# Optimization experiments

Measured on AMD Instinct MI355X. Metric: run time of the kernel, lower is better.

Reference implementation:

```python
import jax, jax.numpy as jnp
import numpy as np

B, L, IN_DIM, D, H, NCONV = 64, 400, 500, 128, 8, 4
HD = D // H  # head dim = 16


def _conv1d(x, w, b, pad, groups=1):
    # x: [B, L, Cin], w: [k, Cin//groups, Cout]
    y = jax.lax.conv_general_dilated(
        x, w, window_strides=(1,), padding=[(pad, pad)],
        dimension_numbers=('NWC', 'WIO', 'NWC'), feature_group_count=groups)
    return y + b


def _layernorm(x, g, b, eps=1e-5):
    mu = jnp.mean(x, axis=-1, keepdims=True)
    var = jnp.mean(jnp.square(x - mu), axis=-1, keepdims=True)
    return (x - mu) * jax.lax.rsqrt(var + eps) * g + b


def _posenc(L, d):
    pos = jnp.arange(L, dtype=jnp.float32)[:, None]                 # [L,1]
    div = jnp.exp(jnp.arange(0, d, 2, dtype=jnp.float32) * (-jnp.log(10000.0) / d))
    ang = pos * div                                                 # [L, d/2]
    return jnp.stack([jnp.sin(ang), jnp.cos(ang)], axis=-1).reshape(L, d)


def setup_inputs() -> dict:
    key = jax.random.key(0)
    ks = jax.random.split(key, 24)
    s = lambda k, shape, scale: jax.random.normal(k, shape, dtype=jnp.float32) * scale
    inp = {
        'x': s(ks[0], (B, L, IN_DIM), 1.0),
        # init conv: k=5, 500 -> 128
        'w_init': s(ks[1], (5, IN_DIM, D), 0.02),
        'b_init': jnp.zeros((D,), jnp.float32),
        # 4 depthwise-separable conv layers (pre-LN, residual): depthwise k=7
        'ln_conv_g': jnp.ones((NCONV, D), jnp.float32),
        'ln_conv_b': jnp.zeros((NCONV, D), jnp.float32),
        'w_dw': s(ks[2], (NCONV, 7, 1, D), 0.1),
        'b_dw': jnp.zeros((NCONV, D), jnp.float32),
        'w_pw': s(ks[3], (NCONV, 1, D, D), 0.05),
        'b_pw': jnp.zeros((NCONV, D), jnp.float32),
        # self-attention (pre-LN, residual)
        'ln_att_g': jnp.ones((D,), jnp.float32),
        'ln_att_b': jnp.zeros((D,), jnp.float32),
        'wq': s(ks[4], (D, D), 0.05), 'bq': jnp.zeros((D,), jnp.float32),
        'wk': s(ks[5], (D, D), 0.05), 'bk': jnp.zeros((D,), jnp.float32),
        'wv': s(ks[6], (D, D), 0.05), 'bv': jnp.zeros((D,), jnp.float32),
        'wo': s(ks[7], (D, D), 0.05), 'bo': jnp.zeros((D,), jnp.float32),
        # FFN (pre-LN, residual)
        'ln_ffn_g': jnp.ones((D,), jnp.float32),
        'ln_ffn_b': jnp.zeros((D,), jnp.float32),
        'w1': s(ks[8], (D, D), 0.05), 'b1': jnp.zeros((D,), jnp.float32),
        'w2': s(ks[9], (D, D), 0.05), 'b2': jnp.zeros((D,), jnp.float32),
    }
    return inp


def reference(x, w_init, b_init, ln_conv_g, ln_conv_b, w_dw, b_dw, w_pw, b_pw,
              ln_att_g, ln_att_b, wq, bq, wk, bk, wv, bv, wo, bo,
              ln_ffn_g, ln_ffn_b, w1, b1, w2, b2):
    # 1) init conv (Conv1d k=5 pad=2, 500 -> 128); torch permutes, equivalent NWC conv
    h = _conv1d(x, w_init, b_init, pad=2)                    # [B, L, D]
    # 2) positional encoding
    h = h + _posenc(h.shape[1], D)
    for i in range(NCONV):
        res = h
        h = _layernorm(h, ln_conv_g[i], ln_conv_b[i])
        h = _conv1d(h, w_dw[i], b_dw[i], pad=3, groups=D)    # depthwise k=7
        h = _conv1d(h, w_pw[i], b_pw[i], pad=0)              # pointwise 1x1
        h = jax.nn.relu(h) + res
    # 4) multi-head self-attention, pre-LN + residual
    res = h
    hn = _layernorm(h, ln_att_g, ln_att_b)
    q = (hn @ wq + bq).reshape(B, L, H, HD)
    k = (hn @ wk + bk).reshape(B, L, H, HD)
    v = (hn @ wv + bv).reshape(B, L, H, HD)
    scores = jnp.einsum('bqhd,bkhd->bhqk', q, k) / jnp.sqrt(jnp.float32(HD))
    attn = jax.nn.softmax(scores, axis=-1)
    o = jnp.einsum('bhqk,bkhd->bqhd', attn, v).reshape(B, L, D)
    h = o @ wo + bo + res
    # 5) FFN, pre-LN + residual
    res = h
    hn = _layernorm(h, ln_ffn_g, ln_ffn_b)
    h = jax.nn.relu(hn @ w1 + b1) @ w2 + b2 + res
    return h
```

## Files before the change

### kernel.cpp

```cpp
#include <hip/hip_runtime.h>
#include <hip/hip_bf16.h>
#include <math.h>

#define B 64
#define L 400
#define IN_DIM 500
#define D 128
#define H 8
#define HD 16
#define NCONV 4
#define BL (B*L)

typedef __attribute__((ext_vector_type(8))) unsigned short ushort8;
typedef __attribute__((ext_vector_type(8))) short bf16x8;
typedef __attribute__((ext_vector_type(4))) float f32x4;

__device__ __forceinline__ unsigned short f2bf(float f) {
    unsigned u = __float_as_uint(f);
    unsigned r = (u + 0x7fffu + ((u >> 16) & 1u)) >> 16;
    return (unsigned short)r;
}
__device__ __forceinline__ float bf2f(unsigned short u) {
    return __uint_as_float(((unsigned)u) << 16);
}

__device__ __forceinline__ void gload16(const void* g, void* l) {
    __builtin_amdgcn_global_load_lds(
        (const __attribute__((address_space(1))) unsigned int*)g,
        (__attribute__((address_space(3))) unsigned int*)l,
        16, 0, 0);
}

__global__ __launch_bounds__(256) void k_cvt_x(
        const float* __restrict__ x, unsigned short* __restrict__ xb) {
    int idx = blockIdx.x * 256 + threadIdx.x;
    int row = idx >> 6, ch = idx & 63;
    int b = row / 404, rr = row - b * 404;
    ushort8 o = (ushort8)0;
    if (rr >= 2 && rr < 402) {
        int l = rr - 2;
        const float* src = x + ((size_t)b * 400 + l) * 500 + ch * 8;
        if (ch < 62) {
            float4 v0 = *(const float4*)(src);
            float4 v1 = *(const float4*)(src + 4);
            o[0] = f2bf(v0.x); o[1] = f2bf(v0.y); o[2] = f2bf(v0.z); o[3] = f2bf(v0.w);
            o[4] = f2bf(v1.x); o[5] = f2bf(v1.y); o[6] = f2bf(v1.z); o[7] = f2bf(v1.w);
        } else {
#pragma unroll
            for (int j = 0; j < 8; ++j) {
                int c = ch * 8 + j;
                o[j] = (c < 500) ? f2bf(src[j]) : (unsigned short)0;
            }
        }
    }
    *(ushort8*)(xb + (size_t)idx * 8) = o;
}

__global__ __launch_bounds__(256) void k_cvt_w(
        const float* __restrict__ w, unsigned short* __restrict__ wbt) {
    int idx = blockIdx.x * 256 + threadIdx.x;
    int k = idx & 511, n = (idx >> 9) & 127, t = idx >> 16;
    float v = (k < 500) ? w[((size_t)t * 500 + k) * 128 + n] : 0.f;
    wbt[idx] = f2bf(v);
}

__global__ __launch_bounds__(256) void k_cvt_wall(
        const float* w0, const float* w1, const float* w2, const float* w3,
        const float* w4, const float* w5, const float* w6, const float* w7,
        const float* w8, const float* w9, unsigned short* __restrict__ out) {
    const float* arr[10] = {w0,w1,w2,w3,w4,w5,w6,w7,w8,w9};
    int widx = blockIdx.x >> 6;
    const float* w = arr[widx];
    int idx = ((blockIdx.x & 63) << 8) + threadIdx.x;
    int n = idx >> 7, k = idx & 127;
    out[(size_t)widx * 16384 + idx] = f2bf(w[k * 128 + n]);
}

#define TM 80
#define BK 64
__global__ __launch_bounds__(256) void k_initconv_mfma(
        const unsigned short* __restrict__ xb,
        const unsigned short* __restrict__ wbt,
        const float* __restrict__ bias, float* __restrict__ out) {
    __shared__ unsigned short As[TM * BK];
    __shared__ unsigned short Ws[64 * BK];
    int tid = threadIdx.x;
    int b = blockIdx.x / 10;
    int rem = blockIdx.x - b * 10;
    int l0 = (rem >> 1) * TM;
    int nh = rem & 1;
    int lane = tid & 63, wave = tid >> 6;
    int kgrp = lane >> 4, lm = lane & 15;

    f32x4 acc[5];
#pragma unroll
    for (int mf = 0; mf < 5; ++mf) acc[mf] = (f32x4)0.f;

    for (int t = 0; t < 5; ++t) {
        const unsigned short* arow = xb + ((size_t)(b * 404 + l0 + t)) * 512;
        const unsigned short* wrow = wbt + (size_t)t * 128 * 512 + (size_t)nh * 64 * 512;
        for (int k0 = 0; k0 < 512; k0 += BK) {
            {
                int idx = tid;
#pragma unroll
                for (int i = 0; i < 2; ++i) {
                    int r = idx >> 3, sc = idx & 7;
                    gload16(arow + (size_t)r * 512 + k0 + ((sc ^ (r & 7)) * 8),
                            As + idx * 8);
                    idx += 256;
                }
                if (idx < 640) {
                    int r = idx >> 3, sc = idx & 7;
                    gload16(arow + (size_t)r * 512 + k0 + ((sc ^ (r & 7)) * 8),
                            As + idx * 8);
                }
            }
#pragma unroll
            for (int i = 0; i < 2; ++i) {
                int idx = tid + i * 256;
                int n = idx >> 3, sc = idx & 7;
                gload16(wrow + (size_t)n * 512 + k0 + ((sc ^ (n & 7)) * 8),
                        Ws + idx * 8);
            }
            __syncthreads();
#pragma unroll
            for (int ks = 0; ks < 2; ++ks) {
                int gc = ks * 4 + kgrp;
                int n = wave * 16 + lm;
                bf16x8 bfr = *(const bf16x8*)(Ws + n * 64 + ((gc ^ (n & 7)) * 8));
#pragma unroll
                for (int mf = 0; mf < 5; ++mf) {
                    int r = mf * 16 + lm;
                    bf16x8 af = *(const bf16x8*)(As + r * 64 + ((gc ^ (r & 7)) * 8));
                    acc[mf] = __builtin_amdgcn_mfma_f32_16x16x32_bf16(
                        af, bfr, acc[mf], 0, 0, 0);
                }
            }
            __syncthreads();
        }
    }

    {
        int n = nh * 64 + wave * 16 + lm;
        float bs = bias[n];
        float pbase = expf(-(float)(n & ~1) * (9.210340371976184f / 128.0f));
#pragma unroll
        for (int mf = 0; mf < 5; ++mf) {
#pragma unroll
            for (int r = 0; r < 4; ++r) {
                int l = l0 + mf * 16 + kgrp * 4 + r;
                float ang = (float)l * pbase;
                float pe = (n & 1) ? cosf(ang) : sinf(ang);
                out[((size_t)b * 400 + l) * 128 + n] = acc[mf][r] + bs + pe;
            }
        }
    }
}

__global__ __launch_bounds__(256) void k_ln(
        const float* __restrict__ in, const float* __restrict__ g,
        const float* __restrict__ bta, unsigned short* __restrict__ out) {
    int wave = threadIdx.x >> 6, lane = threadIdx.x & 63;
    size_t row = (size_t)blockIdx.x * 4 + wave;
    const float* p = in + row * D;
    float2 v = *(const float2*)(p + lane * 2);
    float s = v.x + v.y;
    float q = v.x * v.x + v.y * v.y;
#pragma unroll
    for (int off = 32; off; off >>= 1) {
        s += __shfl_xor(s, off);
        q += __shfl_xor(q, off);
    }
    float mu  = s * (1.f / 128.f);
    float var = q * (1.f / 128.f) - mu * mu;
    float inv = rsqrtf(var + 1e-5f);
    float2 gg = *(const float2*)(g + lane * 2);
    float2 bb = *(const float2*)(bta + lane * 2);
    float ox = (v.x - mu) * inv * gg.x + bb.x;
    float oy = (v.y - mu) * inv * gg.y + bb.y;
    unsigned pk = (unsigned)f2bf(ox) | ((unsigned)f2bf(oy) << 16);
    *(unsigned*)(out + row * D + lane * 2) = pk;
}

__global__ __launch_bounds__(256) void k_dw(
        const unsigned short* __restrict__ in, const float* __restrict__ w,
        const float* __restrict__ bias, unsigned short* __restrict__ out) {
    __shared__ float s[22 * D];
    int tid = threadIdx.x;
    int b  = blockIdx.x / 25;
    int l0 = (blockIdx.x - b * 25) * 16;
    for (int idx = tid; idx < 22 * 16; idx += 256) {
        int r = idx >> 4, c = idx & 15;
        int gl = l0 - 3 + r;
        float vals[8];
        if (gl >= 0 && gl < L) {
            ushort8 u = *(const ushort8*)(in + ((size_t)b * L + gl) * D + c * 8);
#pragma unroll
            for (int j = 0; j < 8; ++j) vals[j] = bf2f(u[j]);
        } else {
#pragma unroll
            for (int j = 0; j < 8; ++j) vals[j] = 0.f;
        }
#pragma unroll
        for (int j = 0; j < 8; ++j) s[r * D + c * 8 + j] = vals[j];
    }
    __syncthreads();
    int d = tid & 127, half = tid >> 7;
    float wr[7];
#pragma unroll
    for (int t = 0; t < 7; ++t) wr[t] = w[t * D + d];
    float bs = bias[d];
    for (int jj = 0; jj < 8; ++jj) {
        int lj = half * 8 + jj;
        float a = bs;
#pragma unroll
        for (int t = 0; t < 7; ++t) a = fmaf(s[(lj + t) * D + d], wr[t], a);
        out[((size_t)b * L + l0 + lj) * D + d] = f2bf(a);
    }
}

__global__ __launch_bounds__(256) void k_gemm_bf16(
        const unsigned short* __restrict__ A,
        const unsigned short* __restrict__ Wt,
        const float* __restrict__ bias,
        const float* __restrict__ res,
        float* __restrict__ outf,
        unsigned short* __restrict__ outb,
        int relu, float oscale) {
    __shared__ unsigned short As[32 * 128];
    __shared__ unsigned short Ws[128 * 128];
    int tid = threadIdx.x;
    int m0 = blockIdx.x * 32;
    int lane = tid & 63, wave = tid >> 6;
    int lm = lane & 15, kgrp = lane >> 4;
    int wm = wave >> 1, wn = wave & 1;

#pragma unroll
    for (int i = 0; i < 2; ++i) {
        int idx = tid + i * 256;
        int r = idx >> 4, sc = idx & 15;
        gload16(A + ((size_t)(m0 + r)) * 128 + ((sc ^ (r & 15)) * 8), As + idx * 8);
    }
#pragma unroll
    for (int i = 0; i < 8; ++i) {
        int idx = tid + i * 256;
        int n = idx >> 4, sc = idx & 15;
        gload16(Wt + ((size_t)n) * 128 + ((sc ^ (n & 15)) * 8), Ws + idx * 8);
    }
    __syncthreads();

    f32x4 acc[4];
#pragma unroll
    for (int nt = 0; nt < 4; ++nt) acc[nt] = (f32x4)0.f;

#pragma unroll
    for (int kc = 0; kc < 4; ++kc) {
        int c = kc * 4 + kgrp;
        int r = wm * 16 + lm;
        bf16x8 af = *(const bf16x8*)(As + (r * 16 + (c ^ (r & 15))) * 8);
#pragma unroll
        for (int nt = 0; nt < 4; ++nt) {
            int n = wn * 64 + nt * 16 + lm;
            bf16x8 bfv = *(const bf16x8*)(Ws + (n * 16 + (c ^ (n & 15))) * 8);
            acc[nt] = __builtin_amdgcn_mfma_f32_16x16x32_bf16(af, bfv, acc[nt], 0, 0, 0);
        }
    }

#pragma unroll
    for (int nt = 0; nt < 4; ++nt) {
        int n = wn * 64 + nt * 16 + lm;
        float bs = bias[n];
#pragma unroll
        for (int r = 0; r < 4; ++r) {
            size_t m = (size_t)m0 + wm * 16 + kgrp * 4 + r;
            float v = acc[nt][r] + bs;
            if (relu) v = fmaxf(v, 0.f);
            if (res)  v += res[m * 128 + n];
            if (outf) outf[m * 128 + n] = v;
            else      outb[m * 128 + n] = f2bf(v * oscale);
        }
    }
}

#define KS 40
#define VS 424
__global__ __launch_bounds__(256) void k_attn_mfma(
        const unsigned short* __restrict__ qb,
        const unsigned short* __restrict__ kb,
        const unsigned short* __restrict__ vb,
        unsigned short* __restrict__ out) {
    __shared__ __align__(16) unsigned short Kpad[400 * KS];
    __shared__ __align__(16) unsigned short Vt[16 * VS];
    __shared__ __align__(16) unsigned short Ptmp[4][16 * KS];
    int tid = threadIdx.x;
    int b = blockIdx.x >> 3, h = blockIdx.x & 7;
    int lane = tid & 63, wave = tid >> 6;
    int lm = lane & 15, kgrp = lane >> 4;

    for (int idx = tid; idx < 800; idx += 256) {
        int l = idx >> 1, half = idx & 1;
        ushort8 kv = *(const ushort8*)(kb + ((size_t)(b * 400 + l)) * 128 + h * 16 + half * 8);
        *(ushort8*)(Kpad + l * KS + half * 8) = kv;
        *(ushort8*)(Kpad + l * KS + 16 + half * 8) = (ushort8)0;
    }
    for (int idx = tid; idx < 800; idx += 256) {
        int kk = idx >> 1, dh = idx & 1;
        ushort8 vv = *(const ushort8*)(vb + ((size_t)(b * 400 + kk)) * 128 + h * 16 + dh * 8);
#pragma unroll
        for (int j = 0; j < 8; ++j) Vt[(dh * 8 + j) * VS + kk] = vv[j];
    }
    {
        int d = tid >> 4, kk = 400 + (tid & 15);
        Vt[d * VS + kk] = 0;
    }
    __syncthreads();

    unsigned short* Pw = Ptmp[wave];
    for (int tt = wave; tt < 25; tt += 4) {
        int q0 = tt * 16;
        bf16x8 Qf = *(const bf16x8*)(qb + ((size_t)(b * 400 + q0 + lm)) * 128 + h * 16 + kgrp * 8);
        f32x4 s[25];
#pragma unroll
        for (int kt = 0; kt < 25; ++kt) {
            bf16x8 Kf = *(const bf16x8*)(Kpad + (kt * 16 + lm) * KS + kgrp * 8);
            s[kt] = __builtin_amdgcn_mfma_f32_16x16x32_bf16(Qf, Kf, (f32x4)0.f, 0, 0, 0);
        }
        float rmax[4], rsum[4];
#pragma unroll
        for (int r = 0; r < 4; ++r) rmax[r] = -1e30f;
#pragma unroll
        for (int kt = 0; kt < 25; ++kt)
#pragma unroll
            for (int r = 0; r < 4; ++r) rmax[r] = fmaxf(rmax[r], s[kt][r]);
#pragma unroll
        for (int mask = 1; mask <= 8; mask <<= 1)
#pragma unroll
            for (int r = 0; r < 4; ++r) rmax[r] = fmaxf(rmax[r], __shfl_xor(rmax[r], mask));
#pragma unroll
        for (int r = 0; r < 4; ++r) rsum[r] = 0.f;
#pragma unroll
        for (int kt = 0; kt < 25; ++kt)
#pragma unroll
            for (int r = 0; r < 4; ++r) {
                float p = __expf(s[kt][r] - rmax[r]);
                s[kt][r] = p;
                rsum[r] += p;
            }
#pragma unroll
        for (int mask = 1; mask <= 8; mask <<= 1)
#pragma unroll
            for (int r = 0; r < 4; ++r) rsum[r] += __shfl_xor(rsum[r], mask);
        float rinv[4];
#pragma unroll
        for (int r = 0; r < 4; ++r) rinv[r] = 1.f / rsum[r];

        f32x4 O = (f32x4)0.f;
#pragma unroll
        for (int kc = 0; kc < 13; ++kc) {
#pragma unroll
            for (int t = 0; t < 2; ++t) {
                int kt = kc * 2 + t;
#pragma unroll
                for (int r = 0; r < 4; ++r) {
                    unsigned short pv = (kt < 25) ? f2bf(s[kt][r]) : (unsigned short)0;
                    Pw[(kgrp * 4 + r) * KS + t * 16 + lm] = pv;
                }
            }
            __builtin_amdgcn_wave_barrier();
            __builtin_amdgcn_s_waitcnt(0);
            __builtin_amdgcn_wave_barrier();
            bf16x8 Pf = *(const bf16x8*)(Pw + lm * KS + kgrp * 8);
            bf16x8 Vf = *(const bf16x8*)(Vt + lm * VS + kc * 32 + kgrp * 8);
            O = __builtin_amdgcn_mfma_f32_16x16x32_bf16(Pf, Vf, O, 0, 0, 0);
            __builtin_amdgcn_wave_barrier();
        }
#pragma unroll
        for (int r = 0; r < 4; ++r) {
            int q = q0 + kgrp * 4 + r;
            out[((size_t)(b * 400 + q)) * 128 + h * 16 + lm] = f2bf(O[r] * rinv[r]);
        }
    }
}

extern "C" void kernel_launch(void* const* d_in, const int* in_sizes, int n_in,
                              void* d_out, int out_size, void* d_ws, size_t ws_size,
                              hipStream_t stream) {
    (void)in_sizes; (void)n_in; (void)out_size; (void)ws_size;
    const float* x      = (const float*)d_in[0];
    const float* w_init = (const float*)d_in[1];
    const float* b_init = (const float*)d_in[2];
    const float* lncg   = (const float*)d_in[3];
    const float* lncb   = (const float*)d_in[4];
    const float* w_dw   = (const float*)d_in[5];
    const float* b_dw   = (const float*)d_in[6];
    const float* w_pw   = (const float*)d_in[7];
    const float* b_pw   = (const float*)d_in[8];
    const float* lnag   = (const float*)d_in[9];
    const float* lnab   = (const float*)d_in[10];
    const float* wq     = (const float*)d_in[11];
    const float* bq     = (const float*)d_in[12];
    const float* wk     = (const float*)d_in[13];
    const float* bk     = (const float*)d_in[14];
    const float* wv     = (const float*)d_in[15];
    const float* bv     = (const float*)d_in[16];
    const float* wo     = (const float*)d_in[17];
    const float* bo     = (const float*)d_in[18];
    const float* lnfg   = (const float*)d_in[19];
    const float* lnfb   = (const float*)d_in[20];
    const float* w1     = (const float*)d_in[21];
    const float* b1     = (const float*)d_in[22];
    const float* w2     = (const float*)d_in[23];
    const float* b2     = (const float*)d_in[24];

    float* ws = (float*)d_ws;
    const size_t NBL = (size_t)BL * D;
    float* h0 = ws;
    float* outp = (float*)d_out;

    unsigned short* hnb = (unsigned short*)(ws + NBL);
    unsigned short* t0b = hnb + NBL;
    unsigned short* qb  = t0b + NBL;
    unsigned short* kb  = qb + NBL;
    unsigned short* vb  = kb + NBL;
    unsigned short* wt  = vb + NBL;
    unsigned short* xb  = wt + 10 * 16384;
    unsigned short* wbt = xb + (size_t)64 * 404 * 512;

    k_cvt_x<<<6464, 256, 0, stream>>>(x, xb);
    k_cvt_w<<<1280, 256, 0, stream>>>(w_init, wbt);
    k_cvt_wall<<<640, 256, 0, stream>>>(
        w_pw, w_pw + 16384, w_pw + 2 * 16384, w_pw + 3 * 16384,
        wq, wk, wv, wo, w1, w2, wt);

    k_initconv_mfma<<<640, 256, 0, stream>>>(xb, wbt, b_init, h0);

    for (int i = 0; i < NCONV; ++i) {
        k_ln<<<6400, 256, 0, stream>>>(h0, lncg + i * D, lncb + i * D, hnb);
        k_dw<<<1600, 256, 0, stream>>>(hnb, w_dw + (size_t)i * 7 * D, b_dw + i * D, t0b);
        k_gemm_bf16<<<800, 256, 0, stream>>>(t0b, wt + (size_t)i * 16384,
                                             b_pw + i * D, h0, h0, nullptr, 1, 1.f);
    }

    k_ln<<<6400, 256, 0, stream>>>(h0, lnag, lnab, hnb);
    k_gemm_bf16<<<800, 256, 0, stream>>>(hnb, wt + 4 * 16384, bq, nullptr,
                                         nullptr, qb, 0, 0.25f);
    k_gemm_bf16<<<800, 256, 0, stream>>>(hnb, wt + 5 * 16384, bk, nullptr,
                                         nullptr, kb, 0, 1.f);
    k_gemm_bf16<<<800, 256, 0, stream>>>(hnb, wt + 6 * 16384, bv, nullptr,
                                         nullptr, vb, 0, 1.f);
    k_attn_mfma<<<512, 256, 0, stream>>>(qb, kb, vb, t0b);
    k_gemm_bf16<<<800, 256, 0, stream>>>(t0b, wt + 7 * 16384, bo, h0,
                                         h0, nullptr, 0, 1.f);

    k_ln<<<6400, 256, 0, stream>>>(h0, lnfg, lnfb, hnb);
    k_gemm_bf16<<<800, 256, 0, stream>>>(hnb, wt + 8 * 16384, b1, nullptr,
                                         nullptr, t0b, 1, 1.f);
    k_gemm_bf16<<<800, 256, 0, stream>>>(t0b, wt + 9 * 16384, b2, h0,
                                         outp, nullptr, 0, 1.f);
}
```

Before: 381.7 us.

## Reuse one 84-row input tile across all five conv taps in init conv

```diff
diff --git a/kernel.cpp b/kernel.cpp
--- a/kernel.cpp
+++ b/kernel.cpp
@@ -82,8 +82,8 @@
         const unsigned short* __restrict__ xb,
         const unsigned short* __restrict__ wbt,
         const float* __restrict__ bias, float* __restrict__ out) {
-    __shared__ unsigned short As[TM * BK];
-    __shared__ unsigned short Ws[64 * BK];
+    __shared__ unsigned short As[84 * BK];
+    __shared__ unsigned short Ws[5][64 * BK];
     int tid = threadIdx.x;
     int b = blockIdx.x / 10;
     int rem = blockIdx.x - b * 10;
@@ -96,48 +96,48 @@
 #pragma unroll
     for (int mf = 0; mf < 5; ++mf) acc[mf] = (f32x4)0.f;
 
-    for (int t = 0; t < 5; ++t) {
-        const unsigned short* arow = xb + ((size_t)(b * 404 + l0 + t)) * 512;
-        const unsigned short* wrow = wbt + (size_t)t * 128 * 512 + (size_t)nh * 64 * 512;
-        for (int k0 = 0; k0 < 512; k0 += BK) {
-            {
-                int idx = tid;
-#pragma unroll
-                for (int i = 0; i < 2; ++i) {
-                    int r = idx >> 3, sc = idx & 7;
-                    gload16(arow + (size_t)r * 512 + k0 + ((sc ^ (r & 7)) * 8),
-                            As + idx * 8);
-                    idx += 256;
-                }
-                if (idx < 640) {
-                    int r = idx >> 3, sc = idx & 7;
-                    gload16(arow + (size_t)r * 512 + k0 + ((sc ^ (r & 7)) * 8),
-                            As + idx * 8);
+    const unsigned short* abase = xb + ((size_t)(b * 404 + l0)) * 512;
+    const unsigned short* wbase = wbt + (size_t)nh * 64 * 512;
+
+    for (int k0 = 0; k0 < 512; k0 += BK) {
+        for (int idx = tid; idx < 672; idx += 256) {
+            int r = idx >> 3, sc = idx & 7;
+            gload16(abase + (size_t)r * 512 + k0 + ((sc ^ (r & 7)) * 8),
+                    As + idx * 8);
+        }
+#pragma unroll
+        for (int i = 0; i < 10; ++i) {
+            int idx = tid + i * 256;
+            int t = idx >> 9;
+            int sub = idx & 511;
+            int n = sub >> 3, sc = sub & 7;
+            gload16(wbase + (size_t)t * 128 * 512 + (size_t)n * 512 + k0
+                        + ((sc ^ (n & 7)) * 8),
+                    &Ws[t][0] + sub * 8);
+        }
+        __syncthreads();
+        int n16 = wave * 16 + lm;
+#pragma unroll
+        for (int ks = 0; ks < 2; ++ks) {
+            int gc = ks * 4 + kgrp;
+            bf16x8 bfr[5];
+#pragma unroll
+            for (int t = 0; t < 5; ++t)
+                bfr[t] = *(const bf16x8*)(&Ws[t][0] + n16 * 64
+                                          + ((gc ^ (n16 & 7)) * 8));
+#pragma unroll
+            for (int mf = 0; mf < 5; ++mf) {
+#pragma unroll
+                for (int t = 0; t < 5; ++t) {
+                    int r = mf * 16 + lm + t;
+                    bf16x8 af = *(const bf16x8*)(As + r * 64
+                                                 + ((gc ^ (r & 7)) * 8));
+                    acc[mf] = __builtin_amdgcn_mfma_f32_16x16x32_bf16(
+                        af, bfr[t], acc[mf], 0, 0, 0);
                 }
             }
-#pragma unroll
-            for (int i = 0; i < 2; ++i) {
-                int idx = tid + i * 256;
-                int n = idx >> 3, sc = idx & 7;
-                gload16(wrow + (size_t)n * 512 + k0 + ((sc ^ (n & 7)) * 8),
-                        Ws + idx * 8);
-            }
-            __syncthreads();
-#pragma unroll
-            for (int ks = 0; ks < 2; ++ks) {
-                int gc = ks * 4 + kgrp;
-                int n = wave * 16 + lm;
-                bf16x8 bfr = *(const bf16x8*)(Ws + n * 64 + ((gc ^ (n & 7)) * 8));
-#pragma unroll
-                for (int mf = 0; mf < 5; ++mf) {
-                    int r = mf * 16 + lm;
-                    bf16x8 af = *(const bf16x8*)(As + r * 64 + ((gc ^ (r & 7)) * 8));
-                    acc[mf] = __builtin_amdgcn_mfma_f32_16x16x32_bf16(
-                        af, bfr, acc[mf], 0, 0, 0);
-                }
-            }
-            __syncthreads();
-        }
+        }
+        __syncthreads();
     }
 
     {
```

New measurement: 362.3 us. 1.05x faster.
